# Kernel tuning notes

Measured on AMD Instinct MI355X. Metric: run time of the kernel, lower is better.

The kernel has to match this reference:

```python
import jax, jax.numpy as jnp
import numpy as np

HIDDEN = 128
HEADS = 8
HEAD_DIM = HIDDEN // HEADS
N_BLOCKS = 2048
N_EDGES = 4096


def setup_inputs() -> dict:
    key = jax.random.key(0)
    ks = jax.random.split(key, 14)
    s = 0.02
    return {
        "block_features": jax.random.normal(ks[0], (N_BLOCKS, HIDDEN), dtype=jnp.float32),
        "edge_indices": jax.random.randint(ks[1], (2, N_EDGES), 0, N_BLOCKS, dtype=jnp.int32),
        # edge_encoder: Linear(2H->H), ReLU, Linear(H->H)
        "W_e1": jax.random.normal(ks[2], (2 * HIDDEN, HIDDEN), dtype=jnp.float32) * s,
        "b_e1": jnp.zeros((HIDDEN,), dtype=jnp.float32),
        "W_e2": jax.random.normal(ks[3], (HIDDEN, HIDDEN), dtype=jnp.float32) * s,
        "b_e2": jnp.zeros((HIDDEN,), dtype=jnp.float32),
        "Wq": jax.random.normal(ks[4], (HIDDEN, HIDDEN), dtype=jnp.float32) * s,
        "bq": jnp.zeros((HIDDEN,), dtype=jnp.float32),
        "Wk": jax.random.normal(ks[5], (HIDDEN, HIDDEN), dtype=jnp.float32) * s,
        "bk": jnp.zeros((HIDDEN,), dtype=jnp.float32),
        "Wv": jax.random.normal(ks[6], (HIDDEN, HIDDEN), dtype=jnp.float32) * s,
        "bv": jnp.zeros((HIDDEN,), dtype=jnp.float32),
        "Wo": jax.random.normal(ks[7], (HIDDEN, HIDDEN), dtype=jnp.float32) * s,
        "bo": jnp.zeros((HIDDEN,), dtype=jnp.float32),
    }


def reference(block_features, edge_indices, W_e1, b_e1, W_e2, b_e2,
              Wq, bq, Wk, bk, Wv, bv, Wo, bo):
    n_blocks = block_features.shape[0]
    src_idx, dst_idx = edge_indices[0], edge_indices[1]

    # gather src/dst node features, concat -> edge MLP (dropout is identity in eval)
    ef = jnp.concatenate([block_features[src_idx], block_features[dst_idx]], axis=1)  # [E, 2H]
    ef = jnp.maximum(ef @ W_e1 + b_e1, 0.0) @ W_e2 + b_e2  # [E, H]

    E = ef.shape[0]
    scale = HEAD_DIM ** -0.5
    q = (ef @ Wq + bq).reshape(E, HEADS, HEAD_DIM)
    k = (ef @ Wk + bk).reshape(E, HEADS, HEAD_DIM)
    v = (ef @ Wv + bv).reshape(E, HEADS, HEAD_DIM)

    # dense attention over all edges
    scores = jnp.einsum("ehd,fhd->hef", q, k) * scale  # [H, E, E]
    attn = jax.nn.softmax(scores, axis=-1)
    attn_out = jnp.einsum("hef,fhd->ehd", attn, v).reshape(E, HIDDEN)
    updated_edges = attn_out @ Wo + bo  # [E, H]

    # scatter_sum back to destination nodes
    block_updates = jax.ops.segment_sum(updated_edges, dst_idx, num_segments=n_blocks)
    return block_features + block_updates
```

## Files before the change

### kernel.cpp

```cpp
#include <hip/hip_runtime.h>
#include <hip/hip_bf16.h>

#define NB 2048
#define NE 4096
#define HID 128
#define NHEAD 8
#define HD 16

#define FPSCALE 1048576.0f
#define INV_FPSCALE (1.0f/1048576.0f)
#define QSCALE 0.36067376022224085f

typedef short s16x8 __attribute__((ext_vector_type(8)));
typedef float f32x4  __attribute__((ext_vector_type(4)));
typedef float f32x16 __attribute__((ext_vector_type(16)));

static __device__ __forceinline__ ushort f2bf(float x) {
    uint u = __builtin_bit_cast(uint, x);
    uint r = (u + 0x7fffu + ((u >> 16) & 1u)) >> 16;
    return (ushort)r;
}
static __device__ __forceinline__ uint pack2bf(float a, float b) {
    return (uint)f2bf(a) | ((uint)f2bf(b) << 16);
}
static __device__ __forceinline__ uint packrd(float a, float b) {
    uint ua = __builtin_bit_cast(uint, a) + 0x8000u;
    uint ub = __builtin_bit_cast(uint, b) + 0x8000u;
    return __builtin_amdgcn_perm(ub, ua, 0x07060302u);
}

__global__ __launch_bounds__(256) void convert_kernel(
    const float* __restrict__ We1, const float* __restrict__ We2,
    const float* __restrict__ Wq,  const float* __restrict__ Wk,
    const float* __restrict__ Wv,  const float* __restrict__ Wo,
    ushort* __restrict__ wb, int4* __restrict__ acc_zero)
{
    int i = blockIdx.x * 256 + threadIdx.x;
    acc_zero[i] = make_int4(0, 0, 0, 0);

    if (i < 8192) {
        int k = i >> 5, n4 = (i & 31) * 4;
        float4 t = *(const float4*)(We1 + k * HID + n4);
        wb[(n4 + 0) * 256 + k] = f2bf(t.x);
        wb[(n4 + 1) * 256 + k] = f2bf(t.y);
        wb[(n4 + 2) * 256 + k] = f2bf(t.z);
        wb[(n4 + 3) * 256 + k] = f2bf(t.w);
    } else if (i < 28672) {
        int j = i - 8192;
        int m = j >> 12;
        int r = j & 4095;
        int k = r >> 5, n4 = (r & 31) * 4;
        const float* W = (m == 0) ? We2 : (m == 1) ? Wq : (m == 2) ? Wk
                       : (m == 3) ? Wv : Wo;
        float4 t = *(const float4*)(W + k * HID + n4);
        ushort* o = wb + 32768 + m * 16384;
        o[(n4 + 0) * 128 + k] = f2bf(t.x);
        o[(n4 + 1) * 128 + k] = f2bf(t.y);
        o[(n4 + 2) * 128 + k] = f2bf(t.z);
        o[(n4 + 3) * 128 + k] = f2bf(t.w);
    }
}

__global__ __launch_bounds__(512, 2) void mlp_qkv_kernel(
    const float* __restrict__ bf, const int* __restrict__ src, const int* __restrict__ dst,
    const ushort* __restrict__ wb,
    const float* __restrict__ be1, const float* __restrict__ be2,
    const float* __restrict__ bq,  const float* __restrict__ bk, const float* __restrict__ bv,
    ushort* __restrict__ qg, ushort* __restrict__ kg, ushort* __restrict__ vT)
{
    __shared__ ushort sX[16][264];
    __shared__ ushort sH[16][136];
    __shared__ ushort sE[16][136];

    const int tid = threadIdx.x;
    const int w   = tid >> 6;
    const int l   = tid & 63;
    const int lo16 = l & 15;
    const int hi4  = l >> 4;
    const int e0 = blockIdx.x * 16;

    const ushort* We1T = wb;
    const ushort* We2T = wb + 32768;
    const ushort* WqT  = wb + 49152;
    const ushort* WkT  = wb + 65536;
    const ushort* WvT  = wb + 81920;

    s16x8 B1[8], B2[4], BQ[4], BK[4], BV[4];
    #pragma unroll
    for (int k0 = 0; k0 < 8; k0++)
        B1[k0] = *(const s16x8*)(We1T + (w * 16 + lo16) * 256 + k0 * 32 + hi4 * 8);
    #pragma unroll
    for (int k0 = 0; k0 < 4; k0++) {
        B2[k0] = *(const s16x8*)(We2T + (w * 16 + lo16) * 128 + k0 * 32 + hi4 * 8);
        BQ[k0] = *(const s16x8*)(WqT  + (w * 16 + lo16) * 128 + k0 * 32 + hi4 * 8);
        BK[k0] = *(const s16x8*)(WkT  + (w * 16 + lo16) * 128 + k0 * 32 + hi4 * 8);
        BV[k0] = *(const s16x8*)(WvT  + (w * 16 + lo16) * 128 + k0 * 32 + hi4 * 8);
    }
    const float bias1 = be1[w * 16 + lo16];
    const float bias2 = be2[w * 16 + lo16];
    const float biasq = bq[w * 16 + lo16];
    const float biask = bk[w * 16 + lo16];
    const float biasv = bv[w * 16 + lo16];

    {
        const int r  = tid >> 5;
        const int sg = tid & 31;
        const int e  = e0 + r;
        const int node = (sg < 16) ? src[e] : dst[e];
        const float4* rowp = (const float4*)(bf + node * HID);
        const int fb = (sg & 15) * 2;
        float4 t0 = rowp[fb], t1 = rowp[fb + 1];
        *(uint2*)&sX[r][sg * 8]     = make_uint2(pack2bf(t0.x, t0.y), pack2bf(t0.z, t0.w));
        *(uint2*)&sX[r][sg * 8 + 4] = make_uint2(pack2bf(t1.x, t1.y), pack2bf(t1.z, t1.w));
    }
    __syncthreads();

    f32x4 acc;

    {
        acc = (f32x4){bias1, bias1, bias1, bias1};
        #pragma unroll
        for (int k0 = 0; k0 < 8; k0++) {
            s16x8 a = *(const s16x8*)&sX[lo16][k0 * 32 + hi4 * 8];
            acc = __builtin_amdgcn_mfma_f32_16x16x32_bf16(a, B1[k0], acc, 0, 0, 0);
        }
        #pragma unroll
        for (int r = 0; r < 4; r++)
            sH[hi4 * 4 + r][w * 16 + lo16] = f2bf(fmaxf(acc[r], 0.0f));
    }
    __syncthreads();

    {
        acc = (f32x4){bias2, bias2, bias2, bias2};
        #pragma unroll
        for (int k0 = 0; k0 < 4; k0++) {
            s16x8 a = *(const s16x8*)&sH[lo16][k0 * 32 + hi4 * 8];
            acc = __builtin_amdgcn_mfma_f32_16x16x32_bf16(a, B2[k0], acc, 0, 0, 0);
        }
        #pragma unroll
        for (int r = 0; r < 4; r++)
            sE[hi4 * 4 + r][w * 16 + lo16] = f2bf(acc[r]);
    }
    __syncthreads();

#define PROJ(BARR, BIAS, STORE) do { \
    acc = (f32x4){BIAS, BIAS, BIAS, BIAS}; \
    _Pragma("unroll") \
    for (int k0 = 0; k0 < 4; k0++) { \
        s16x8 a = *(const s16x8*)&sE[lo16][k0 * 32 + hi4 * 8]; \
        acc = __builtin_amdgcn_mfma_f32_16x16x32_bf16(a, BARR[k0], acc, 0, 0, 0); \
    } \
    _Pragma("unroll") \
    for (int r = 0; r < 4; r++) { STORE; } \
} while (0)

    PROJ(BQ, biasq, { int e = e0 + hi4 * 4 + r;
                      qg[(w * NE + e) * 16 + lo16] = f2bf(acc[r] * QSCALE); });
    PROJ(BK, biask, { int e = e0 + hi4 * 4 + r;
                      kg[(w * NE + e) * 16 + lo16] = f2bf(acc[r]); });
    PROJ(BV, biasv, { int e = e0 + hi4 * 4 + r;
                      vT[(w * 16 + lo16) * NE + e] = f2bf(acc[r]); });
#undef PROJ
}

__global__ __launch_bounds__(512) void attn_kernel(
    const ushort* __restrict__ qg, const ushort* __restrict__ kg,
    const ushort* __restrict__ vT, ushort* __restrict__ Og)
{
    __shared__ ushort Pbuf[8][2048];

    const int tid = threadIdx.x;
    const int w   = tid >> 6;
    const int l   = tid & 63;
    const int h   = blockIdx.y;
    const int q0  = blockIdx.x * 32;
    const int lo16 = l & 15, hi4 = l >> 4;
    const int lo32 = l & 31, hi2 = l >> 5;

    ushort* Pw = &Pbuf[w][0];

    const s16x8 qf = *(const s16x8*)(qg + (h * NE + q0 + lo32) * 16 + hi2 * 8);
    const s16x8 ones = __builtin_bit_cast(s16x8,
        make_uint4(0x3f803f80u, 0x3f803f80u, 0x3f803f80u, 0x3f803f80u));

    const f32x16 z16 = {};
    f32x4 o0 = {0,0,0,0}, o1 = {0,0,0,0};
    f32x4 l0 = {0,0,0,0}, l1 = {0,0,0,0};

    const int kbase = w * (NE / 8);
    const ushort* kp = kg + (size_t)h * NE * 16;
    const ushort* vp = vT + (size_t)(h * 16 + lo16) * NE;

    s16x8 kf = *(const s16x8*)(kp + (kbase + lo32) * 16 + hi2 * 8);
    s16x8 vf = *(const s16x8*)(vp + kbase + hi4 * 8);

    #pragma unroll 2
    for (int kt = 0; kt < 16; kt++) {
        const s16x8 kc = kf, vc = vf;
        const int key1 = kbase + ((kt + 1) & 15) * 32;
        kf = *(const s16x8*)(kp + (key1 + lo32) * 16 + hi2 * 8);
        vf = *(const s16x8*)(vp + key1 + hi4 * 8);

        f32x16 s = __builtin_amdgcn_mfma_f32_32x32x16_bf16(kc, qf, z16, 0, 0, 0);

        const int b8 = (kt & 1) * 8;
        #pragma unroll
        for (int g = 0; g < 4; g++) {
            uint2 w2 = make_uint2(
                packrd(__builtin_amdgcn_exp2f(s[4*g]),   __builtin_amdgcn_exp2f(s[4*g+1])),
                packrd(__builtin_amdgcn_exp2f(s[4*g+2]), __builtin_amdgcn_exp2f(s[4*g+3])));
            *(uint2*)&Pw[((b8 + 2*g + hi2) * 32 + lo32) * 4] = w2;
        }

        uint2 alo = *(const uint2*)&Pw[((b8 + 2*hi4)     * 32 + lo16) * 4];
        uint2 ahi = *(const uint2*)&Pw[((b8 + 2*hi4 + 1) * 32 + lo16) * 4];
        uint2 blo = *(const uint2*)&Pw[((b8 + 2*hi4)     * 32 + 16 + lo16) * 4];
        uint2 bhi = *(const uint2*)&Pw[((b8 + 2*hi4 + 1) * 32 + 16 + lo16) * 4];
        s16x8 pb0 = __builtin_bit_cast(s16x8, make_uint4(alo.x, alo.y, ahi.x, ahi.y));
        s16x8 pb1 = __builtin_bit_cast(s16x8, make_uint4(blo.x, blo.y, bhi.x, bhi.y));

        o0 = __builtin_amdgcn_mfma_f32_16x16x32_bf16(vc, pb0, o0, 0, 0, 0);
        o1 = __builtin_amdgcn_mfma_f32_16x16x32_bf16(vc, pb1, o1, 0, 0, 0);
        l0 = __builtin_amdgcn_mfma_f32_16x16x32_bf16(ones, pb0, l0, 0, 0, 0);
        l1 = __builtin_amdgcn_mfma_f32_16x16x32_bf16(ones, pb1, l1, 0, 0, 0);
    }

    __syncthreads();
    float* sO = (float*)&Pbuf[0][0];
    #pragma unroll
    for (int r = 0; r < 4; r++) {
        sO[(w * 32 + lo16) * 18 + hi4 * 4 + r]      = o0[r];
        sO[(w * 32 + 16 + lo16) * 18 + hi4 * 4 + r] = o1[r];
    }
    if (hi4 == 0) {
        sO[(w * 32 + lo16) * 18 + 16]      = l0[0];
        sO[(w * 32 + 16 + lo16) * 18 + 16] = l1[0];
    }
    __syncthreads();

    {
        const int q = tid >> 4;
        const int d = tid & 15;
        float sum = 0.0f, Lq = 0.0f;
        #pragma unroll
        for (int ww = 0; ww < 8; ww++) {
            sum += sO[(ww * 32 + q) * 18 + d];
            Lq  += sO[(ww * 32 + q) * 18 + 16];
        }
        Og[(q0 + q) * HID + h * 16 + d] = f2bf(sum / Lq);
    }
}

__global__ __launch_bounds__(512, 2) void wo_scatter_kernel(
    const ushort* __restrict__ Og, const ushort* __restrict__ wb,
    const float* __restrict__ bo, const int* __restrict__ dst,
    int* __restrict__ acc_int)
{
    const int tid = threadIdx.x;
    const int w   = tid >> 6;
    const int l   = tid & 63;
    const int lo16 = l & 15, hi4 = l >> 4;
    const int e0 = blockIdx.x * 16;
    const ushort* WoT = wb + 98304;

    s16x8 BO[4], AO[4];
    #pragma unroll
    for (int k0 = 0; k0 < 4; k0++) {
        BO[k0] = *(const s16x8*)(WoT + (w * 16 + lo16) * 128 + k0 * 32 + hi4 * 8);
        AO[k0] = *(const s16x8*)(Og + (e0 + lo16) * HID + k0 * 32 + hi4 * 8);
    }
    int dste[4];
    #pragma unroll
    for (int r = 0; r < 4; r++) dste[r] = dst[e0 + hi4 * 4 + r];
    const float b_ = bo[w * 16 + lo16];

    f32x4 acc = (f32x4){b_, b_, b_, b_};
    #pragma unroll
    for (int k0 = 0; k0 < 4; k0++)
        acc = __builtin_amdgcn_mfma_f32_16x16x32_bf16(AO[k0], BO[k0], acc, 0, 0, 0);

    #pragma unroll
    for (int r = 0; r < 4; r++) {
        atomicAdd(acc_int + dste[r] * HID + w * 16 + lo16,
                  __float2int_rn(acc[r] * FPSCALE));
    }
}

__global__ __launch_bounds__(256) void finalize_kernel(
    const float4* __restrict__ bf, const int4* __restrict__ acc_int,
    float4* __restrict__ out)
{
    int i = blockIdx.x * 256 + threadIdx.x;
    float4 b = bf[i];
    int4   a = acc_int[i];
    out[i] = make_float4(b.x + (float)a.x * INV_FPSCALE,
                         b.y + (float)a.y * INV_FPSCALE,
                         b.z + (float)a.z * INV_FPSCALE,
                         b.w + (float)a.w * INV_FPSCALE);
}

extern "C" void kernel_launch(void* const* d_in, const int* in_sizes, int n_in,
                              void* d_out, int out_size, void* d_ws, size_t ws_size,
                              hipStream_t stream)
{
    const float* bf  = (const float*)d_in[0];
    const int*   ei  = (const int*)d_in[1];
    const int*   src = ei;
    const int*   dst = ei + NE;
    const float* We1 = (const float*)d_in[2];
    const float* be1 = (const float*)d_in[3];
    const float* We2 = (const float*)d_in[4];
    const float* be2 = (const float*)d_in[5];
    const float* Wq  = (const float*)d_in[6];
    const float* bq  = (const float*)d_in[7];
    const float* Wk  = (const float*)d_in[8];
    const float* bk  = (const float*)d_in[9];
    const float* Wv  = (const float*)d_in[10];
    const float* bv  = (const float*)d_in[11];
    const float* Wo  = (const float*)d_in[12];
    const float* bo  = (const float*)d_in[13];

    char* ws = (char*)d_ws;
    ushort* wb  = (ushort*)(ws);
    ushort* qg  = (ushort*)(ws + (1u<<18));
    ushort* kg  = (ushort*)(ws + (1u<<18) + (1u<<20));
    ushort* vT  = (ushort*)(ws + (1u<<18) + (2u<<20));
    ushort* Og  = (ushort*)(ws + (1u<<18) + (3u<<20));
    int*   acc  = (int*)  (ws + (1u<<18) + (4u<<20));

    convert_kernel<<<256, 256, 0, stream>>>(We1, We2, Wq, Wk, Wv, Wo, wb, (int4*)acc);
    mlp_qkv_kernel<<<NE / 16, 512, 0, stream>>>(bf, src, dst, wb, be1, be2, bq, bk, bv,
                                                qg, kg, vT);
    attn_kernel<<<dim3(NE / 32, NHEAD), 512, 0, stream>>>(qg, kg, vT, Og);
    wo_scatter_kernel<<<NE / 16, 512, 0, stream>>>(Og, wb, bo, dst, acc);
    finalize_kernel<<<(NB * HID) / 1024, 256, 0, stream>>>((const float4*)bf, (const int4*)acc,
                                                           (float4*)d_out);
}
```

Baseline: 51.87 us.

## Scatter with float atomics directly into output and drop finalize kernel

The output is initialised with block_features inside the MLP kernel, and the Wo projection scatters with float atomicAdd straight into the output. This removes the fixed-point int accumulator, its zeroing in the convert kernel, and the separate finalize launch, so the convert grid shrinks to the blocks needed for weight conversion. The trade-offs are a nondeterministic float summation order and reliance on hardware float atomics instead of integer ones.

```diff
diff --git a/kernel.cpp b/kernel.cpp
--- a/kernel.cpp
+++ b/kernel.cpp
@@ -7,8 +7,6 @@
 #define NHEAD 8
 #define HD 16
 
-#define FPSCALE 1048576.0f
-#define INV_FPSCALE (1.0f/1048576.0f)
 #define QSCALE 0.36067376022224085f
 
 typedef short s16x8 __attribute__((ext_vector_type(8)));
@@ -33,11 +31,9 @@
     const float* __restrict__ We1, const float* __restrict__ We2,
     const float* __restrict__ Wq,  const float* __restrict__ Wk,
     const float* __restrict__ Wv,  const float* __restrict__ Wo,
-    ushort* __restrict__ wb, int4* __restrict__ acc_zero)
+    ushort* __restrict__ wb)
 {
     int i = blockIdx.x * 256 + threadIdx.x;
-    acc_zero[i] = make_int4(0, 0, 0, 0);
-
     if (i < 8192) {
         int k = i >> 5, n4 = (i & 31) * 4;
         float4 t = *(const float4*)(We1 + k * HID + n4);
@@ -66,7 +62,8 @@
     const ushort* __restrict__ wb,
     const float* __restrict__ be1, const float* __restrict__ be2,
     const float* __restrict__ bq,  const float* __restrict__ bk, const float* __restrict__ bv,
-    ushort* __restrict__ qg, ushort* __restrict__ kg, ushort* __restrict__ vT)
+    ushort* __restrict__ qg, ushort* __restrict__ kg, ushort* __restrict__ vT,
+    float4* __restrict__ out_init)
 {
     __shared__ ushort sX[16][264];
     __shared__ ushort sH[16][136];
@@ -78,6 +75,9 @@
     const int lo16 = l & 15;
     const int hi4  = l >> 4;
     const int e0 = blockIdx.x * 16;
+
+    if (tid < 256)
+        out_init[blockIdx.x * 256 + tid] = ((const float4*)bf)[blockIdx.x * 256 + tid];
 
     const ushort* We1T = wb;
     const ushort* We2T = wb + 32768;
@@ -254,7 +254,7 @@
 __global__ __launch_bounds__(512, 2) void wo_scatter_kernel(
     const ushort* __restrict__ Og, const ushort* __restrict__ wb,
     const float* __restrict__ bo, const int* __restrict__ dst,
-    int* __restrict__ acc_int)
+    float* __restrict__ out)
 {
     const int tid = threadIdx.x;
     const int w   = tid >> 6;
@@ -281,22 +281,8 @@
 
     #pragma unroll
     for (int r = 0; r < 4; r++) {
-        atomicAdd(acc_int + dste[r] * HID + w * 16 + lo16,
-                  __float2int_rn(acc[r] * FPSCALE));
-    }
-}
-
-__global__ __launch_bounds__(256) void finalize_kernel(
-    const float4* __restrict__ bf, const int4* __restrict__ acc_int,
-    float4* __restrict__ out)
-{
-    int i = blockIdx.x * 256 + threadIdx.x;
-    float4 b = bf[i];
-    int4   a = acc_int[i];
-    out[i] = make_float4(b.x + (float)a.x * INV_FPSCALE,
-                         b.y + (float)a.y * INV_FPSCALE,
-                         b.z + (float)a.z * INV_FPSCALE,
-                         b.w + (float)a.w * INV_FPSCALE);
+        atomicAdd(out + dste[r] * HID + w * 16 + lo16, acc[r]);
+    }
 }
 
 extern "C" void kernel_launch(void* const* d_in, const int* in_sizes, int n_in,
@@ -326,13 +312,10 @@
     ushort* kg  = (ushort*)(ws + (1u<<18) + (1u<<20));
     ushort* vT  = (ushort*)(ws + (1u<<18) + (2u<<20));
     ushort* Og  = (ushort*)(ws + (1u<<18) + (3u<<20));
-    int*   acc  = (int*)  (ws + (1u<<18) + (4u<<20));
-
-    convert_kernel<<<256, 256, 0, stream>>>(We1, We2, Wq, Wk, Wv, Wo, wb, (int4*)acc);
+
+    convert_kernel<<<112, 256, 0, stream>>>(We1, We2, Wq, Wk, Wv, Wo, wb);
     mlp_qkv_kernel<<<NE / 16, 512, 0, stream>>>(bf, src, dst, wb, be1, be2, bq, bk, bv,
-                                                qg, kg, vT);
+                                                qg, kg, vT, (float4*)d_out);
     attn_kernel<<<dim3(NE / 32, NHEAD), 512, 0, stream>>>(qg, kg, vT, Og);
-    wo_scatter_kernel<<<NE / 16, 512, 0, stream>>>(Og, wb, bo, dst, acc);
-    finalize_kernel<<<(NB * HID) / 1024, 256, 0, stream>>>((const float4*)bf, (const int4*)acc,
-                                                           (float4*)d_out);
-}
+    wo_scatter_kernel<<<NE / 16, 512, 0, stream>>>(Og, wb, bo, dst, (float*)d_out);
+}
```

New measurement: 50.65 us. 1.02x faster.
